# Performance work log

Hardware: AMD Instinct MI355X
Metric: run time of the kernel (lower is better)

## Reference

```python
import jax, jax.numpy as jnp
import numpy as np

N = 25000   # nodes
M = 150000  # edges
D = 512     # d_Embedding
H = 8       # heads
DK = 64     # per-head key dim
DV = 64     # per-head value dim


def setup_inputs() -> dict:
    key = jax.random.key(0)
    ks = jax.random.split(key, 8)
    x = jax.random.normal(ks[0], (N, D), jnp.float32)
    edge_index = jax.random.randint(ks[1], (2, M), 0, N).astype(jnp.int32)
    s_in = 1.0 / np.sqrt(D).astype(np.float32)   # fan-in scaling like nn.Linear init
    s_ff = 1.0 / np.sqrt(H * DV).astype(np.float32)
    Wk = jax.random.normal(ks[2], (D, H * DK), jnp.float32) * s_in
    Wq = jax.random.normal(ks[3], (D, H * DK), jnp.float32) * s_in
    Wv = jax.random.normal(ks[4], (D, H * DV), jnp.float32) * s_in
    Wff = jax.random.normal(ks[5], (H * DV, D), jnp.float32) * s_ff
    bk = jnp.zeros((H * DK,), jnp.float32)
    bq = jnp.zeros((H * DK,), jnp.float32)
    bv = jnp.zeros((H * DV,), jnp.float32)
    bff = jnp.zeros((D,), jnp.float32)
    return {"x": x, "edge_index": edge_index, "Wk": Wk, "bk": bk,
            "Wq": Wq, "bq": bq, "Wv": Wv, "bv": bv, "Wff": Wff, "bff": bff}


def reference(x, edge_index, Wk, bk, Wq, bq, Wv, bv, Wff, bff):
    # Q/K/V projections with per-head reshape (make_heads)
    K = (x @ Wk + bk).reshape(-1, H, DK)
    Q = (x @ Wq + bq).reshape(-1, H, DK)
    V = (x @ Wv + bv).reshape(-1, H, DV)
    senders, receivers = edge_index[0], edge_index[1]
    # edge scores: (M, H)
    att = jnp.einsum('mhd,mhd->mh', Q[receivers], K[senders]) / np.sqrt(DK).astype(np.float32)
    att = jnp.exp(att + 3.0 - att.max())  # global-max-shifted exp, as in source
    # normalize by sum of incoming strengths per receiver node (segment softmax denom)
    ssum = jax.ops.segment_sum(att, receivers, num_segments=N)  # (N, H)
    denom = ssum[receivers]
    att = jnp.where(denom == 0, 0.0, att / jnp.where(denom == 0, 1.0, denom))
    # weighted message + scatter-add aggregate: (N, H, DV)
    msg = att[..., None] * V[senders]
    agg = jax.ops.segment_sum(msg, receivers, num_segments=N)
    # aggregate_heads: Linear over concatenated heads
    return agg.reshape(-1, H * DV) @ Wff + bff
```

## Files before the change

### kernel.cpp

```cpp
#include <hip/hip_runtime.h>
#include <hip/hip_bf16.h>

#define DMODEL 512

typedef __attribute__((ext_vector_type(8))) short bf16x8;
typedef __attribute__((ext_vector_type(4))) float f32x4;

__device__ inline void gload_lds16(const void* g, void* s) {
  __builtin_amdgcn_global_load_lds((const __attribute__((address_space(1))) void*)g,
                                   (__attribute__((address_space(3))) void*)s, 16, 0, 0);
}

__device__ inline float bflo(unsigned u) {
  union { float f; unsigned u; } c; c.u = u << 16; return c.f;
}
__device__ inline float bfhi(unsigned u) {
  union { float f; unsigned u; } c; c.u = u & 0xffff0000u; return c.f;
}

template <bool OUT_BF16, int NT>
__global__ __launch_bounds__(512, 2)
void gemm_quad(const __hip_bfloat16* __restrict__ Ap,
               const __hip_bfloat16* __restrict__ Wp,
               const float* __restrict__ bias, void* __restrict__ Cv,
               int Nrows, int ncols) {
  __shared__ __align__(16) short sA[32768];
  const int tid = threadIdx.x;
  const int lane = tid & 63, w = tid >> 6;
  const int q = blockIdx.x;
  const __hip_bfloat16* Aq = Ap + (size_t)q * 32768;

#pragma unroll
  for (int i = 0; i < 8; ++i)
    gload_lds16(Aq + (size_t)(i * 512 + tid) * 8, &sA[(i * 512 + tid) * 8]);
  __syncthreads();

  const int l15 = lane & 15, lq = lane >> 4;

#pragma unroll 1
  for (int gs = 0; gs < NT / 4; ++gs) {
    const int ntb = w * NT + gs * 4;
    const __hip_bfloat16* Wb = Wp + (size_t)ntb * 16 * 512 + lane * 8;
    f32x4 acc[4][4] = {};
    bf16x8 b_cur[4], b_nxt[4];
#pragma unroll
    for (int n = 0; n < 4; ++n)
      b_cur[n] = *(const bf16x8*)(Wb + (size_t)(n * 16) * 512);

#pragma unroll 1
    for (int c = 0; c < 16; ++c) {
      if (c < 15) {
#pragma unroll
        for (int n = 0; n < 4; ++n)
          b_nxt[n] = *(const bf16x8*)(Wb + (size_t)(n * 16 + c + 1) * 512);
      }
#pragma unroll
      for (int m = 0; m < 4; ++m) {
        bf16x8 af = *(const bf16x8*)&sA[(m * 16 + c) * 512 + lane * 8];
#pragma unroll
        for (int n = 0; n < 4; ++n)
          acc[m][n] = __builtin_amdgcn_mfma_f32_16x16x32_bf16(af, b_cur[n], acc[m][n], 0, 0, 0);
      }
      if (c < 15) {
#pragma unroll
        for (int n = 0; n < 4; ++n) b_cur[n] = b_nxt[n];
      }
    }

#pragma unroll
    for (int m = 0; m < 4; ++m) {
      int rowb = q * 64 + m * 16;
#pragma unroll
      for (int n = 0; n < 4; ++n) {
        int col = (ntb + n) * 16 + l15;
        float bv = bias[col];
#pragma unroll
        for (int i = 0; i < 4; ++i) {
          int row = rowb + lq * 4 + i;
          if (row < Nrows) {
            float v = acc[m][n][i] + bv;
            if (OUT_BF16)
              ((__hip_bfloat16*)Cv)[(size_t)row * ncols + col] = __float2bfloat16(v);
            else
              ((float*)Cv)[(size_t)row * ncols + col] = v;
          }
        }
      }
    }
  }
}

__global__ void cvtp_kernel(const float* __restrict__ x, __hip_bfloat16* __restrict__ xp,
                            int Nrows, int NpadRows) {
  int tid = blockIdx.x * 256 + threadIdx.x;
  int r = tid >> 6, kb = tid & 63;
  if (r >= NpadRows) return;
  int t = r >> 4, c = kb >> 2, qq = kb & 3, lp = qq * 16 + (r & 15);
  __hip_bfloat16* dst = xp + (size_t)t * 8192 + c * 512 + lp * 8;
  union { ushort4 u[2]; __hip_bfloat16 h[8]; } o;
#pragma unroll
  for (int j = 0; j < 8; ++j) o.h[j] = __float2bfloat16(0.f);
  if (r < Nrows) {
    float4 v0 = *(const float4*)(x + (size_t)r * DMODEL + kb * 8);
    float4 v1 = *(const float4*)(x + (size_t)r * DMODEL + kb * 8 + 4);
    o.h[0] = __float2bfloat16(v0.x); o.h[1] = __float2bfloat16(v0.y);
    o.h[2] = __float2bfloat16(v0.z); o.h[3] = __float2bfloat16(v0.w);
    o.h[4] = __float2bfloat16(v1.x); o.h[5] = __float2bfloat16(v1.y);
    o.h[6] = __float2bfloat16(v1.z); o.h[7] = __float2bfloat16(v1.w);
  }
  *(ushort4*)dst = o.u[0];
  *(ushort4*)(dst + 4) = o.u[1];
}

__global__ __launch_bounds__(256)
void wp_kernel(const float* __restrict__ Wk, const float* __restrict__ Wq,
               const float* __restrict__ Wv, const float* __restrict__ Wff,
               __hip_bfloat16* __restrict__ Wp_qkv, __hip_bfloat16* __restrict__ Wp_ff) {
  int c = blockIdx.x;
  int S = blockIdx.y;
  const float* W; __hip_bfloat16* dst;
  if (S < 8)       { W = Wk;  dst = Wp_qkv + (size_t)S * 32768; }
  else if (S < 16) { W = Wq;  dst = Wp_qkv + (size_t)S * 32768; }
  else if (S < 24) { W = Wv;  dst = Wp_qkv + (size_t)S * 32768; }
  else             { W = Wff; dst = Wp_ff + (size_t)(S - 24) * 32768; }
  int colbase = (S & 7) * 64;
  __shared__ float tile[32][64];
  for (int idx = threadIdx.x; idx < 2048; idx += 256) {
    int r = idx >> 6, col = idx & 63;
    tile[r][col] = W[(size_t)(c * 32 + r) * DMODEL + colbase + col];
  }
  __syncthreads();
  int n = threadIdx.x >> 6, l = threadIdx.x & 63;
  union { ushort4 u[2]; __hip_bfloat16 h[8]; } o;
#pragma unroll
  for (int j = 0; j < 8; ++j)
    o.h[j] = __float2bfloat16(tile[(l >> 4) * 8 + j][n * 16 + (l & 15)]);
  __hip_bfloat16* p = dst + ((size_t)(n * 16 + c) * 64 + l) * 8;
  *(ushort4*)p = o.u[0];
  *(ushort4*)(p + 4) = o.u[1];
}

__global__ void bias_kernel(const float* __restrict__ bk, const float* __restrict__ bq,
                            const float* __restrict__ bv, float* __restrict__ o) {
  int i = blockIdx.x * 256 + threadIdx.x;
  if (i < 512) o[i] = bk[i];
  else if (i < 1024) o[i] = bq[i - 512];
  else if (i < 1536) o[i] = bv[i - 1024];
}

__global__ void hist_kernel(const int* __restrict__ recv, int* __restrict__ deg, int M_) {
  int m = blockIdx.x * 256 + threadIdx.x;
  if (m < M_) atomicAdd(&deg[recv[m]], 1);
}

__global__ __launch_bounds__(256)
void scan_block(const int* __restrict__ deg, int* __restrict__ offs,
                int* __restrict__ bsum, int n) {
  __shared__ int sd[256];
  const int t = threadIdx.x;
  const int base = blockIdx.x * 1024;
  int v[4], s = 0;
#pragma unroll
  for (int j = 0; j < 4; ++j) {
    int idx = base + t * 4 + j;
    v[j] = (idx < n) ? deg[idx] : 0;
    s += v[j];
  }
  sd[t] = s;
  __syncthreads();
  for (int off = 1; off < 256; off <<= 1) {
    int x = (t >= off) ? sd[t - off] : 0;
    __syncthreads();
    sd[t] += x;
    __syncthreads();
  }
  int run = sd[t] - s;
#pragma unroll
  for (int j = 0; j < 4; ++j) {
    int idx = base + t * 4 + j;
    if (idx < n) offs[idx] = run;
    run += v[j];
  }
  if (t == 255) bsum[blockIdx.x] = sd[255];
}

__global__ void scan_mid(const int* __restrict__ bsum, int* __restrict__ bbase,
                         int nb, int* __restrict__ offs, int n) {
  int t = threadIdx.x;
  int x = (t < nb) ? bsum[t] : 0;
  int v = x;
  for (int off = 1; off < 64; off <<= 1) {
    int y = __shfl_up(v, off);
    if (t >= off) v += y;
  }
  if (t < nb) bbase[t] = v - x;
  if (t == nb - 1) offs[n] = v;
}

__global__ void scan_add(int* __restrict__ offs, const int* __restrict__ bbase,
                         int* __restrict__ cursor, int n) {
  int i = blockIdx.x * 256 + threadIdx.x;
  if (i < n) {
    int o = offs[i] + bbase[i >> 10];
    offs[i] = o;
    cursor[i] = o;
  }
}

__global__ void fill_kernel(const int* __restrict__ senders, const int* __restrict__ recv,
                            int* __restrict__ cursor, int* __restrict__ sidx, int M_) {
  int m = blockIdx.x * 256 + threadIdx.x;
  if (m < M_) {
    int pos = atomicAdd(&cursor[recv[m]], 1);
    sidx[pos] = senders[m];
  }
}

__global__ __launch_bounds__(256)
void attn_kernel(const __hip_bfloat16* __restrict__ QKV, const int* __restrict__ sidx,
                 const int* __restrict__ offs, __hip_bfloat16* __restrict__ aggp, int n) {
  const int lane = threadIdx.x & 63;
  const int wid  = threadIdx.x >> 6;
  const int r = blockIdx.x * 4 + wid;
  if (r >= n) return;
  const int start = offs[r];
  const int end   = offs[r + 1];

  uint4 qr = *(const uint4*)(QKV + (size_t)r * 1536 + 512 + lane * 8);
  float q[8] = {bflo(qr.x), bfhi(qr.x), bflo(qr.y), bfhi(qr.y),
                bflo(qr.z), bfhi(qr.z), bflo(qr.w), bfhi(qr.w)};

  float ssum = 0.f;
  float acc[8] = {};
  int e = start;
  for (; e + 2 <= end; e += 2) {
    int s0 = sidx[e], s1 = sidx[e + 1];
    const __hip_bfloat16* p0 = QKV + (size_t)s0 * 1536 + lane * 8;
    const __hip_bfloat16* p1 = QKV + (size_t)s1 * 1536 + lane * 8;
    uint4 k0 = *(const uint4*)p0;
    uint4 v0 = *(const uint4*)(p0 + 1024);
    uint4 k1 = *(const uint4*)p1;
    uint4 v1 = *(const uint4*)(p1 + 1024);
    float d0 = q[0] * bflo(k0.x) + q[1] * bfhi(k0.x) + q[2] * bflo(k0.y) + q[3] * bfhi(k0.y)
             + q[4] * bflo(k0.z) + q[5] * bfhi(k0.z) + q[6] * bflo(k0.w) + q[7] * bfhi(k0.w);
    float d1 = q[0] * bflo(k1.x) + q[1] * bfhi(k1.x) + q[2] * bflo(k1.y) + q[3] * bfhi(k1.y)
             + q[4] * bflo(k1.z) + q[5] * bfhi(k1.z) + q[6] * bflo(k1.w) + q[7] * bfhi(k1.w);
    d0 += __shfl_xor(d0, 1); d1 += __shfl_xor(d1, 1);
    d0 += __shfl_xor(d0, 2); d1 += __shfl_xor(d1, 2);
    d0 += __shfl_xor(d0, 4); d1 += __shfl_xor(d1, 4);
    float w0 = expf(d0 * 0.125f), w1 = expf(d1 * 0.125f);
    ssum += w0 + w1;
    acc[0] += w0 * bflo(v0.x) + w1 * bflo(v1.x);
    acc[1] += w0 * bfhi(v0.x) + w1 * bfhi(v1.x);
    acc[2] += w0 * bflo(v0.y) + w1 * bflo(v1.y);
    acc[3] += w0 * bfhi(v0.y) + w1 * bfhi(v1.y);
    acc[4] += w0 * bflo(v0.z) + w1 * bflo(v1.z);
    acc[5] += w0 * bfhi(v0.z) + w1 * bfhi(v1.z);
    acc[6] += w0 * bflo(v0.w) + w1 * bflo(v1.w);
    acc[7] += w0 * bfhi(v0.w) + w1 * bfhi(v1.w);
  }
  if (e < end) {
    int s0 = sidx[e];
    const __hip_bfloat16* p0 = QKV + (size_t)s0 * 1536 + lane * 8;
    uint4 k0 = *(const uint4*)p0;
    uint4 v0 = *(const uint4*)(p0 + 1024);
    float d0 = q[0] * bflo(k0.x) + q[1] * bfhi(k0.x) + q[2] * bflo(k0.y) + q[3] * bfhi(k0.y)
             + q[4] * bflo(k0.z) + q[5] * bfhi(k0.z) + q[6] * bflo(k0.w) + q[7] * bfhi(k0.w);
    d0 += __shfl_xor(d0, 1);
    d0 += __shfl_xor(d0, 2);
    d0 += __shfl_xor(d0, 4);
    float w0 = expf(d0 * 0.125f);
    ssum += w0;
    acc[0] += w0 * bflo(v0.x); acc[1] += w0 * bfhi(v0.x);
    acc[2] += w0 * bflo(v0.y); acc[3] += w0 * bfhi(v0.y);
    acc[4] += w0 * bflo(v0.z); acc[5] += w0 * bfhi(v0.z);
    acc[6] += w0 * bflo(v0.w); acc[7] += w0 * bfhi(v0.w);
  }
  const float inv = (end > start) ? 1.0f / ssum : 0.f;
  union { ushort4 u[2]; __hip_bfloat16 h[8]; } o;
#pragma unroll
  for (int j = 0; j < 8; ++j) o.h[j] = __float2bfloat16(acc[j] * inv);
  int t = r >> 4, c = lane >> 2, qq = lane & 3, lp = qq * 16 + (r & 15);
  __hip_bfloat16* dst = aggp + (size_t)t * 8192 + c * 512 + lp * 8;
  *(ushort4*)dst = o.u[0];
  *(ushort4*)(dst + 4) = o.u[1];
}

extern "C" void kernel_launch(void* const* d_in, const int* in_sizes, int n_in,
                              void* d_out, int out_size, void* d_ws, size_t ws_size,
                              hipStream_t stream) {
  const float* x    = (const float*)d_in[0];
  const int*   eidx = (const int*)d_in[1];
  const float* Wk   = (const float*)d_in[2];
  const float* bk   = (const float*)d_in[3];
  const float* Wq   = (const float*)d_in[4];
  const float* bq   = (const float*)d_in[5];
  const float* Wv   = (const float*)d_in[6];
  const float* bv   = (const float*)d_in[7];
  const float* Wff  = (const float*)d_in[8];
  const float* bff  = (const float*)d_in[9];
  float* out = (float*)d_out;

  const int N_ = in_sizes[0] / DMODEL;
  const int M_ = in_sizes[1] / 2;
  const int* senders = eidx;
  const int* recv    = eidx + M_;

  const int T16 = (N_ + 15) / 16;
  const int Q4  = (T16 + 3) / 4;
  const int Npad = Q4 * 64;

  __hip_bfloat16* xp    = (__hip_bfloat16*)d_ws;
  __hip_bfloat16* QKVb  = xp + (size_t)Npad * DMODEL;
  __hip_bfloat16* aggp  = QKVb + (size_t)N_ * 1536;
  __hip_bfloat16* Wp_qkv = aggp + (size_t)Npad * DMODEL;
  __hip_bfloat16* Wp_ff  = Wp_qkv + (size_t)24 * 32768;
  float* bqkv = (float*)(Wp_ff + (size_t)8 * 32768);
  int* deg    = (int*)(bqkv + 1536);
  int* offs   = deg + N_;
  int* cursor = offs + N_ + 1;
  int* sidx   = cursor + N_;
  int* bsum   = sidx + M_;
  int* bbase  = bsum + 64;

  const int nblk = (N_ + 1023) / 1024;

  cvtp_kernel<<<(Npad * 64 + 255) / 256, 256, 0, stream>>>(x, xp, N_, Npad);
  wp_kernel<<<dim3(16, 32), 256, 0, stream>>>(Wk, Wq, Wv, Wff, Wp_qkv, Wp_ff);
  bias_kernel<<<6, 256, 0, stream>>>(bk, bq, bv, bqkv);

  hipMemsetAsync(deg, 0, N_ * sizeof(int), stream);
  hist_kernel<<<(M_ + 255) / 256, 256, 0, stream>>>(recv, deg, M_);
  scan_block<<<nblk, 256, 0, stream>>>(deg, offs, bsum, N_);
  scan_mid<<<1, 64, 0, stream>>>(bsum, bbase, nblk, offs, N_);
  scan_add<<<(N_ + 255) / 256, 256, 0, stream>>>(offs, bbase, cursor, N_);
  fill_kernel<<<(M_ + 255) / 256, 256, 0, stream>>>(senders, recv, cursor, sidx, M_);

  gemm_quad<true, 12><<<Q4, 512, 0, stream>>>(xp, Wp_qkv, bqkv, QKVb, N_, 1536);

  attn_kernel<<<(N_ + 3) / 4, 256, 0, stream>>>(QKVb, sidx, offs, aggp, N_);

  gemm_quad<false, 4><<<Q4, 512, 0, stream>>>(aggp, Wp_ff, bff, out, N_, DMODEL);
}
```

Baseline: 313.1 us.

## Reorder packed weight layout, triple-buffer B loads, nontemporal stores, raise occupancy hint

Several changes are made to the GEMM. The packed weight layout is reordered so that the four 16-column tiles for each k-chunk sit contiguously, making the B loads denser. The B fragments are prefetched two chunks ahead through a three-slot rotation in a fully unrolled k loop, and the min-blocks launch bound is raised from 2 to 4. The LDS staging load also gets a cache-policy bit, and outputs are written with nontemporal stores. The higher occupancy target and full unroll may add register pressure or spills, and nontemporal stores could hurt the downstream gather kernels if they now miss in cache.

```diff
diff --git a/kernel.cpp b/kernel.cpp
--- a/kernel.cpp
+++ b/kernel.cpp
@@ -8,7 +8,7 @@
 
 __device__ inline void gload_lds16(const void* g, void* s) {
   __builtin_amdgcn_global_load_lds((const __attribute__((address_space(1))) void*)g,
-                                   (__attribute__((address_space(3))) void*)s, 16, 0, 0);
+                                   (__attribute__((address_space(3))) void*)s, 16, 0, 2);
 }
 
 __device__ inline float bflo(unsigned u) {
@@ -19,7 +19,7 @@
 }
 
 template <bool OUT_BF16, int NT>
-__global__ __launch_bounds__(512, 2)
+__global__ __launch_bounds__(512, 4)
 void gemm_quad(const __hip_bfloat16* __restrict__ Ap,
                const __hip_bfloat16* __restrict__ Wp,
                const float* __restrict__ bias, void* __restrict__ Cv,
@@ -40,30 +40,33 @@
 #pragma unroll 1
   for (int gs = 0; gs < NT / 4; ++gs) {
     const int ntb = w * NT + gs * 4;
-    const __hip_bfloat16* Wb = Wp + (size_t)ntb * 16 * 512 + lane * 8;
+    const int stripe = w * (NT / 4) + gs;
+    const __hip_bfloat16* Wb = Wp + (size_t)stripe * 32768 + lane * 8;
     f32x4 acc[4][4] = {};
-    bf16x8 b_cur[4], b_nxt[4];
+    bf16x8 b[3][4];
+
 #pragma unroll
     for (int n = 0; n < 4; ++n)
-      b_cur[n] = *(const bf16x8*)(Wb + (size_t)(n * 16) * 512);
-
-#pragma unroll 1
+      b[0][n] = *(const bf16x8*)(Wb + (size_t)(0 * 4 + n) * 512);
+#pragma unroll
+    for (int n = 0; n < 4; ++n)
+      b[1][n] = *(const bf16x8*)(Wb + (size_t)(1 * 4 + n) * 512);
+
+#pragma unroll
     for (int c = 0; c < 16; ++c) {
-      if (c < 15) {
+      if (c + 2 < 16) {
+        const int slot = (c + 2) % 3;
 #pragma unroll
         for (int n = 0; n < 4; ++n)
-          b_nxt[n] = *(const bf16x8*)(Wb + (size_t)(n * 16 + c + 1) * 512);
+          b[slot][n] = *(const bf16x8*)(Wb + (size_t)((c + 2) * 4 + n) * 512);
       }
+      const int cs = c % 3;
 #pragma unroll
       for (int m = 0; m < 4; ++m) {
         bf16x8 af = *(const bf16x8*)&sA[(m * 16 + c) * 512 + lane * 8];
 #pragma unroll
         for (int n = 0; n < 4; ++n)
-          acc[m][n] = __builtin_amdgcn_mfma_f32_16x16x32_bf16(af, b_cur[n], acc[m][n], 0, 0, 0);
-      }
-      if (c < 15) {
-#pragma unroll
-        for (int n = 0; n < 4; ++n) b_cur[n] = b_nxt[n];
+          acc[m][n] = __builtin_amdgcn_mfma_f32_16x16x32_bf16(af, b[cs][n], acc[m][n], 0, 0, 0);
       }
     }
 
@@ -79,10 +82,14 @@
           int row = rowb + lq * 4 + i;
           if (row < Nrows) {
             float v = acc[m][n][i] + bv;
-            if (OUT_BF16)
-              ((__hip_bfloat16*)Cv)[(size_t)row * ncols + col] = __float2bfloat16(v);
-            else
-              ((float*)Cv)[(size_t)row * ncols + col] = v;
+            if (OUT_BF16) {
+              __hip_bfloat16 hv = __float2bfloat16(v);
+              unsigned short us;
+              __builtin_memcpy(&us, &hv, 2);
+              __builtin_nontemporal_store(us, (unsigned short*)Cv + (size_t)row * ncols + col);
+            } else {
+              __builtin_nontemporal_store(v, (float*)Cv + (size_t)row * ncols + col);
+            }
           }
         }
       }
@@ -135,7 +142,7 @@
 #pragma unroll
   for (int j = 0; j < 8; ++j)
     o.h[j] = __float2bfloat16(tile[(l >> 4) * 8 + j][n * 16 + (l & 15)]);
-  __hip_bfloat16* p = dst + ((size_t)(n * 16 + c) * 64 + l) * 8;
+  __hip_bfloat16* p = dst + ((size_t)(c * 4 + n) * 64 + l) * 8;
   *(ushort4*)p = o.u[0];
   *(ushort4*)(p + 4) = o.u[1];
 }
```

New measurement: 559.1 us. +78.6%, slower.
